# Performance work log

Measured on AMD Instinct MI355X. Metric: run time of the kernel, lower is better.

## Reference

```python
import jax, jax.numpy as jnp
import numpy as np

WINDOW = (7, 7)
SHIFT = (3, 3)
NUM_HEADS = 4
DIM = 128


def _rel_pos_index():
    wh, ww = WINDOW
    coords = np.stack(np.meshgrid(np.arange(wh), np.arange(ww), indexing='ij'))  # [2,wh,ww]
    cf = coords.reshape(2, -1)                    # [2, N]
    rc = (cf[:, :, None] - cf[:, None, :]).transpose(1, 2, 0)  # [N,N,2]
    rc[:, :, 0] += wh - 1
    rc[:, :, 1] += ww - 1
    rc[:, :, 0] *= 2 * ww - 1
    return jnp.asarray(rc.sum(-1).reshape(-1))    # [N*N] int


def _attn_mask_np(pH, pW, sh):
    # Static-shape shift mask (host-side numpy; constant under jit).
    wh, ww = WINDOW
    m = np.zeros((pH, pW))
    h_slices = ((0, pH - wh), (pH - wh, pH - sh[0]), (pH - sh[0], pH))
    w_slices = ((0, pW - ww), (pW - ww, pW - sh[1]), (pW - sh[1], pW))
    cnt = 0
    for hs in h_slices:
        for ws in w_slices:
            m[hs[0]:hs[1], ws[0]:ws[1]] = cnt
            cnt += 1
    m = m.reshape(pH // wh, wh, pW // ww, ww).transpose(0, 2, 1, 3).reshape(-1, wh * ww)
    diff = m[:, None, :] - m[:, :, None]          # [num_windows, N, N]
    return jnp.asarray(np.where(diff != 0, -100.0, 0.0), dtype=np.float32)


def setup_inputs() -> dict:
    key = jax.random.key(0)
    ks = jax.random.split(key, 9)
    B, H, W, C = 32, 56, 56, DIM
    return {
        'input_q': jax.random.normal(ks[0], (B, H, W, C), jnp.float32),
        'input_k': jax.random.normal(ks[1], (B, H, W, C), jnp.float32),
        'input_v': jax.random.normal(ks[2], (B, H, W, C), jnp.float32),
        'q_weight': jax.random.normal(ks[3], (C, C), jnp.float32) * 0.05,
        'q_bias': jnp.zeros((C,), jnp.float32),
        'k_weight': jax.random.normal(ks[4], (C, C), jnp.float32) * 0.05,
        'k_bias': jnp.zeros((C,), jnp.float32),
        'v_weight': jax.random.normal(ks[5], (C, C), jnp.float32) * 0.05,
        'v_bias': jnp.zeros((C,), jnp.float32),
        'proj_weight': jax.random.normal(ks[6], (C, C), jnp.float32) * 0.05,
        'proj_bias': jnp.zeros((C,), jnp.float32),
        'rpb_table': jax.random.normal(ks[7], ((2 * WINDOW[0] - 1) * (2 * WINDOW[1] - 1), NUM_HEADS), jnp.float32) * 0.02,
    }


def reference(input_q, input_k, input_v, q_weight, q_bias, k_weight, k_bias,
              v_weight, v_bias, proj_weight, proj_bias, rpb_table):
    B, H, W, C = input_q.shape
    wh, ww = WINDOW
    pad_b = (wh - H % wh) % wh
    pad_r = (ww - W % ww) % ww
    pad = lambda t: jnp.pad(t, ((0, 0), (0, pad_b), (0, pad_r), (0, 0)))
    qx, kx, vx = pad(input_q), pad(input_k), pad(input_v)
    pad_H, pad_W = H + pad_b, W + pad_r
    sh = [0 if wh >= pad_H else SHIFT[0], 0 if ww >= pad_W else SHIFT[1]]
    if sum(sh) > 0:
        roll = lambda t: jnp.roll(t, (-sh[0], -sh[1]), axis=(1, 2))
        qx, kx, vx = roll(qx), roll(kx), roll(vx)
    nWh, nWw = pad_H // wh, pad_W // ww
    num_windows = nWh * nWw
    N = wh * ww

    def part(t):  # [B,pH,pW,C] -> [B*num_windows, N, C]
        t = t.reshape(B, nWh, wh, nWw, ww, C).transpose(0, 1, 3, 2, 4, 5)
        return t.reshape(B * num_windows, N, C)

    qx, kx, vx = part(qx), part(kx), part(vx)
    hd = C // NUM_HEADS

    def heads(x, w, b):  # linear + split heads -> [BW, nH, N, hd]
        return (x @ w.T + b).reshape(-1, N, NUM_HEADS, hd).transpose(0, 2, 1, 3)

    q = heads(qx, q_weight, q_bias) * (hd ** -0.5)
    k = heads(kx, k_weight, k_bias)
    v = heads(vx, v_weight, v_bias)

    attn = jnp.einsum('whqd,whkd->whqk', q, k)    # [BW, nH, N, N]
    rpb = rpb_table[_rel_pos_index()].reshape(N, N, NUM_HEADS).transpose(2, 0, 1)[None]
    attn = attn + rpb
    if sum(sh) > 0:
        mask = _attn_mask_np(pad_H, pad_W, sh)    # [num_windows, N, N]
        attn = attn.reshape(B, num_windows, NUM_HEADS, N, N) + mask[None, :, None]
        attn = attn.reshape(B * num_windows, NUM_HEADS, N, N)
    attn = jax.nn.softmax(attn, axis=-1)

    x = jnp.einsum('whqk,whkd->whqd', attn, v).transpose(0, 2, 1, 3).reshape(B * num_windows, N, C)
    x = x @ proj_weight.T + proj_bias
    x = x.reshape(B, nWh, nWw, wh, ww, C).transpose(0, 1, 3, 2, 4, 5).reshape(B, pad_H, pad_W, C)
    if sum(sh) > 0:
        x = jnp.roll(x, (sh[0], sh[1]), axis=(1, 2))
    return x[:, :H, :W, :]
```

## Files before the change

kernel.cpp:

```cpp
#include <hip/hip_runtime.h>
#include <hip/hip_bf16.h>

typedef __attribute__((ext_vector_type(8))) short s16x8;
typedef __attribute__((ext_vector_type(4))) float f32x4;
typedef __attribute__((ext_vector_type(16))) float f32x16;
typedef __attribute__((ext_vector_type(2))) unsigned int u32x2;
typedef __attribute__((ext_vector_type(4))) unsigned int u32x4;

#define MFMA16(a, b, c) __builtin_amdgcn_mfma_f32_16x16x32_bf16((a), (b), (c), 0, 0, 0)
#define MFMA32(a, b, c) __builtin_amdgcn_mfma_f32_32x32x16_bf16((a), (b), (c), 0, 0, 0)
#define LOG2E 1.4426950408889634f

static __device__ __forceinline__ unsigned int pk2(float a, float b) {
  union { __hip_bfloat162 h2; unsigned int u; } cv;
  cv.h2 = __float22bfloat162_rn(make_float2(a, b));
  return cv.u;
}
static __device__ __forceinline__ int div7(int x) { return (x * 9363) >> 16; }
static __device__ __forceinline__ int swz256(int row, int byteoff) {
  return row * 256 + (byteoff ^ ((row & 7) << 4));
}
static __device__ __forceinline__ int swz128(int row, int byteoff) {
  return row * 128 + (byteoff ^ ((row & 7) << 4));
}

__global__ void swin_prep(const float* __restrict__ wq, const float* __restrict__ wk,
                          const float* __restrict__ wv, const float* __restrict__ wp,
                          const float* __restrict__ rpb_table,
                          unsigned short* __restrict__ wsW, float* __restrict__ rpbm) {
  int idx = blockIdx.x * 256 + threadIdx.x;
  if (idx < 65536) {
    int t = idx >> 14, loc = idx & 16383;
    const float* s = (t == 0) ? wq : (t == 1) ? wk : (t == 2) ? wv : wp;
    union { __hip_bfloat16 h; unsigned short u; } cv;
    cv.h = __float2bfloat16(s[loc]);
    wsW[idx] = cv.u;
  } else {
    int k = idx - 65536;
    int c = k >> 14;
    int h = (k >> 12) & 3;
    int i = (k >> 6) & 63, j = k & 63;
    float val;
    if (j >= 49) val = -1e30f;
    else if (i >= 49) val = 0.f;
    else {
      int yi = div7(i), xi = i - yi * 7;
      int yj = div7(j), xj = j - yj * 7;
      int ridx = (yi - yj + 6) * 13 + (xi - xj + 6);
      val = rpb_table[ridx * 4 + h];
      int cwi = c >> 1, cwj = c & 1;
      int rgi = (cwi ? (yi < 4 ? 3 : 6) : 0) + (cwj ? (xi < 4 ? 1 : 2) : 0);
      int rgj = (cwi ? (yj < 4 ? 3 : 6) : 0) + (cwj ? (xj < 4 ? 1 : 2) : 0);
      if (rgi != rgj) val -= 100.f;
      val *= LOG2E;
    }
    rpbm[k] = val;
  }
}

__global__ __launch_bounds__(512, 6) void swin_main(
    const float* __restrict__ xq, const float* __restrict__ xk, const float* __restrict__ xv,
    const float* __restrict__ bq, const float* __restrict__ bk, const float* __restrict__ bv,
    const float* __restrict__ bp, const unsigned short* __restrict__ wsW,
    const float* __restrict__ rpbm, float* __restrict__ out) {
  __shared__ __align__(16) char sm[49152];

  const int tid = threadIdx.x;
  const int lane = tid & 63;
  const int wv_ = tid >> 6;
  const int l15 = lane & 15;
  const int lg = lane >> 4;
  const int kgrp = lg * 8;
  const int rsub = lg * 4;
  const int l31 = lane & 31;
  const int hi = lane >> 5;

  const int bid = blockIdx.x;
  const int b = bid >> 6;
  const int widx = bid & 63;
  const int wi = widx >> 3, wj = widx & 7;
  const long obase = (long)b * 56 * 56 * 128;
  const int mcase = ((wi == 7) ? 2 : 0) + ((wj == 7) ? 1 : 0);

  const int xrow = tid >> 3;
  const int xk16 = (tid & 7) << 4;
  long xoff = -1;
  if (xrow < 49) {
    int ty = div7(xrow), tx = xrow - ty * 7;
    int ih = wi * 7 + ty + 3; if (ih >= 56) ih -= 56;
    int iw = wj * 7 + tx + 3; if (iw >= 56) iw -= 56;
    xoff = obase + (long)((ih * 56 + iw) * 128 + xk16);
  }
  float xr[16];
#pragma unroll
  for (int i = 0; i < 16; ++i) xr[i] = 0.f;

  auto issue_x = [&](const float* src) {
    if (xoff >= 0) {
      const float* p = src + xoff;
#pragma unroll
      for (int q = 0; q < 4; ++q) {
        f32x4 v = *(const f32x4*)(p + q * 4);
        xr[q * 4 + 0] = v[0]; xr[q * 4 + 1] = v[1];
        xr[q * 4 + 2] = v[2]; xr[q * 4 + 3] = v[3];
      }
    }
  };
  auto write_x = [&]() {
    unsigned int w[8];
#pragma unroll
    for (int i = 0; i < 8; ++i) w[i] = pk2(xr[2 * i], xr[2 * i + 1]);
    u32x4 a = {w[0], w[1], w[2], w[3]};
    u32x4 bb = {w[4], w[5], w[6], w[7]};
    *(u32x4*)(sm + swz256(xrow, xk16 * 2)) = a;
    *(u32x4*)(sm + swz256(xrow, xk16 * 2 + 16)) = bb;
  };

  auto linearT = [&](int woff, const float* bias, float scale, int dstbase) {
    const int nrow = wv_ * 16 + l15;
    s16x8 afr[4];
#pragma unroll
    for (int kt = 0; kt < 4; ++kt)
      afr[kt] = *(const s16x8*)(wsW + woff + nrow * 128 + kt * 32 + kgrp);
    f32x4 bv4 = *(const f32x4*)(bias + wv_ * 16 + rsub);
    float bb0 = bv4[0] * scale, bb1 = bv4[1] * scale;
    float bb2 = bv4[2] * scale, bb3 = bv4[3] * scale;
#pragma unroll
    for (int tt = 0; tt < 4; ++tt) {
      f32x4 acc = {0.f, 0.f, 0.f, 0.f};
#pragma unroll
      for (int kt = 0; kt < 4; ++kt) {
        s16x8 bfr = *(const s16x8*)(sm + swz256(tt * 16 + l15, (kt * 32 + kgrp) * 2));
        acc = MFMA16(afr[kt], bfr, acc);
      }
      u32x2 pkw = {pk2(acc[0] * scale + bb0, acc[1] * scale + bb1),
                   pk2(acc[2] * scale + bb2, acc[3] * scale + bb3)};
      *(u32x2*)(sm + dstbase + swz256(tt * 16 + l15, 2 * (wv_ * 16 + rsub))) = pkw;
    }
  };

  auto linearV = [&](int woff, const float* bias) {
    const int n = wv_ * 16 + l15;
    s16x8 bfr[4];
#pragma unroll
    for (int kt = 0; kt < 4; ++kt)
      bfr[kt] = *(const s16x8*)(wsW + woff + n * 128 + kt * 32 + kgrp);
    float bval = bias[n];
#pragma unroll
    for (int mt = 0; mt < 4; ++mt) {
      f32x4 acc = {0.f, 0.f, 0.f, 0.f};
#pragma unroll
      for (int kt = 0; kt < 4; ++kt) {
        s16x8 afr = *(const s16x8*)(sm + swz256(mt * 16 + l15, (kt * 32 + kgrp) * 2));
        acc = MFMA16(afr, bfr[kt], acc);
      }
      u32x2 pkw = {pk2(acc[0] + bval, acc[1] + bval), pk2(acc[2] + bval, acc[3] + bval)};
      *(u32x2*)(sm + 16384 + swz128(n, 2 * (mt * 16 + rsub))) = pkw;
    }
  };

  const float QSCALE = 0.17677669529663687f * LOG2E;

  issue_x(xq);
  write_x(); __syncthreads();
  issue_x(xk);
  linearT(0, bq, QSCALE, 16384); __syncthreads();
  write_x(); __syncthreads();
  issue_x(xv);
  linearT(16384, bk, 1.f, 32768); __syncthreads();
  write_x();

  const int h = wv_ & 3;
  const int half = wv_ >> 2;
  const int coff = h * 32;
  unsigned int pu[2][4][2];
  {
    s16x8 qfr[2], kfr[2][2];
#pragma unroll
    for (int s = 0; s < 2; ++s) {
      qfr[s] = *(const s16x8*)(sm + 16384 + swz256(half * 32 + l31, 2 * (coff + s * 16 + hi * 8)));
#pragma unroll
      for (int t = 0; t < 2; ++t)
        kfr[t][s] = *(const s16x8*)(sm + 32768 + swz256(t * 32 + l31, 2 * (coff + s * 16 + hi * 8)));
    }
    f32x16 S[2];
    S[0] = (f32x16)0.f; S[1] = (f32x16)0.f;
#pragma unroll
    for (int s = 0; s < 2; ++s) {
      S[0] = MFMA32(kfr[0][s], qfr[s], S[0]);
      S[1] = MFMA32(kfr[1][s], qfr[s], S[1]);
    }
    const float* rpbm_h = rpbm + (((mcase << 2) + h) << 12) + (half * 32 + l31) * 64 + 4 * hi;
#pragma unroll
    for (int t = 0; t < 2; ++t)
#pragma unroll
      for (int g = 0; g < 4; ++g) {
        f32x4 rv = *(const f32x4*)(rpbm_h + t * 32 + g * 8);
#pragma unroll
        for (int e = 0; e < 4; ++e) S[t][g * 4 + e] += rv[e];
      }
    float m = S[0][0];
#pragma unroll
    for (int t = 0; t < 2; ++t)
#pragma unroll
      for (int r = 0; r < 16; ++r) m = fmaxf(m, S[t][r]);
    m = fmaxf(m, __shfl_xor(m, 32));
    float sum = 0.f;
#pragma unroll
    for (int t = 0; t < 2; ++t)
#pragma unroll
      for (int r = 0; r < 16; ++r) { float e = exp2f(S[t][r] - m); S[t][r] = e; sum += e; }
    sum += __shfl_xor(sum, 32);
    float inv = 1.0f / sum;
#pragma unroll
    for (int t = 0; t < 2; ++t)
#pragma unroll
      for (int g = 0; g < 4; ++g) {
        pu[t][g][0] = pk2(S[t][g * 4 + 0] * inv, S[t][g * 4 + 1] * inv);
        pu[t][g][1] = pk2(S[t][g * 4 + 2] * inv, S[t][g * 4 + 3] * inv);
      }
  }
  __syncthreads();
  linearV(32768, bv);
  __syncthreads();

  {
    f32x16 O = (f32x16)0.f;
#pragma unroll
    for (int s = 0; s < 4; ++s) {
      const int t = s >> 1, gb = (s & 1) * 2;
      unsigned int own0 = pu[t][gb + hi][0], own1 = pu[t][gb + hi][1];
      unsigned int po0 = __shfl_xor(pu[t][gb + 1 - hi][0], 32);
      unsigned int po1 = __shfl_xor(pu[t][gb + 1 - hi][1], 32);
      union { u32x4 u; s16x8 s; } pf;
      pf.u = hi ? (u32x4){po0, po1, own0, own1} : (u32x4){own0, own1, po0, po1};
      s16x8 vfr = *(const s16x8*)(sm + 16384 + swz128(coff + l31, 2 * (s * 16 + hi * 8)));
      O = MFMA32(vfr, pf.s, O);
    }
#pragma unroll
    for (int g = 0; g < 4; ++g) {
      u32x2 w = {pk2(O[g * 4 + 0], O[g * 4 + 1]), pk2(O[g * 4 + 2], O[g * 4 + 3])};
      *(u32x2*)(sm + 32768 + swz256(half * 32 + l31, 2 * (coff + g * 8 + 4 * hi))) = w;
    }
  }
  __syncthreads();

  {
    const int nrow = wv_ * 16 + l15;
    s16x8 afr[4];
#pragma unroll
    for (int kt = 0; kt < 4; ++kt)
      afr[kt] = *(const s16x8*)(wsW + 49152 + nrow * 128 + kt * 32 + kgrp);
    f32x4 bv4 = *(const f32x4*)(bp + wv_ * 16 + rsub);
#pragma unroll
    for (int tt = 0; tt < 4; ++tt) {
      f32x4 acc = {0.f, 0.f, 0.f, 0.f};
#pragma unroll
      for (int kt = 0; kt < 4; ++kt) {
        s16x8 bfr = *(const s16x8*)(sm + 32768 + swz256(tt * 16 + l15, (kt * 32 + kgrp) * 2));
        acc = MFMA16(afr[kt], bfr, acc);
      }
      int tok = tt * 16 + l15;
      if (tok < 49) {
        int ty = div7(tok), tx = tok - ty * 7;
        int oh = wi * 7 + ty + 3; if (oh >= 56) oh -= 56;
        int ow = wj * 7 + tx + 3; if (ow >= 56) ow -= 56;
        f32x4 res = {acc[0] + bv4[0], acc[1] + bv4[1], acc[2] + bv4[2], acc[3] + bv4[3]};
        *(f32x4*)(out + obase + (oh * 56 + ow) * 128 + wv_ * 16 + rsub) = res;
      }
    }
  }
}

extern "C" void kernel_launch(void* const* d_in, const int* in_sizes, int n_in,
                              void* d_out, int out_size, void* d_ws, size_t ws_size,
                              hipStream_t stream) {
  const float* xq = (const float*)d_in[0];
  const float* xk = (const float*)d_in[1];
  const float* xv = (const float*)d_in[2];
  const float* wq = (const float*)d_in[3];
  const float* bq = (const float*)d_in[4];
  const float* wk = (const float*)d_in[5];
  const float* bk = (const float*)d_in[6];
  const float* wv = (const float*)d_in[7];
  const float* bv = (const float*)d_in[8];
  const float* wp = (const float*)d_in[9];
  const float* bp = (const float*)d_in[10];
  const float* rpb = (const float*)d_in[11];

  unsigned short* wsW = (unsigned short*)d_ws;
  float* rpbm = (float*)((char*)d_ws + 131072);

  swin_prep<<<512, 256, 0, stream>>>(wq, wk, wv, wp, rpb, wsW, rpbm);

  float* out = (float*)d_out;
  swin_main<<<2048, 512, 0, stream>>>(xq, xk, xv, bq, bk, bv, bp, wsW, rpbm, out);
}
```

Before: 87.01 us.

## Load Q/K/V inputs together and compute all projections before a single barrier

All three input tiles (q, k, v) are now loaded from global memory up front and staged into separate LDS regions, replacing the earlier sequence of load/project/sync per tensor. The three linear projections run back-to-back with their results held in registers, then are written to LDS after one barrier. The bias-table load is issued before the QK MFMA so it can seed the accumulator, and the V projection no longer sits between softmax and the PV product. This cuts the number of block-wide barriers and exposes more memory-level parallelism, at the cost of higher register pressure and possibly lower occupancy.

```diff
diff --git a/kernel.cpp b/kernel.cpp
--- a/kernel.cpp
+++ b/kernel.cpp
@@ -91,114 +91,149 @@
     int iw = wj * 7 + tx + 3; if (iw >= 56) iw -= 56;
     xoff = obase + (long)((ih * 56 + iw) * 128 + xk16);
   }
-  float xr[16];
-#pragma unroll
-  for (int i = 0; i < 16; ++i) xr[i] = 0.f;
-
-  auto issue_x = [&](const float* src) {
+  {
+    float ra[16], rb[16], rc[16];
+#pragma unroll
+    for (int i = 0; i < 16; ++i) { ra[i] = 0.f; rb[i] = 0.f; rc[i] = 0.f; }
     if (xoff >= 0) {
-      const float* p = src + xoff;
 #pragma unroll
       for (int q = 0; q < 4; ++q) {
-        f32x4 v = *(const f32x4*)(p + q * 4);
-        xr[q * 4 + 0] = v[0]; xr[q * 4 + 1] = v[1];
-        xr[q * 4 + 2] = v[2]; xr[q * 4 + 3] = v[3];
-      }
-    }
-  };
-  auto write_x = [&]() {
-    unsigned int w[8];
-#pragma unroll
-    for (int i = 0; i < 8; ++i) w[i] = pk2(xr[2 * i], xr[2 * i + 1]);
-    u32x4 a = {w[0], w[1], w[2], w[3]};
-    u32x4 bb = {w[4], w[5], w[6], w[7]};
-    *(u32x4*)(sm + swz256(xrow, xk16 * 2)) = a;
-    *(u32x4*)(sm + swz256(xrow, xk16 * 2 + 16)) = bb;
-  };
-
-  auto linearT = [&](int woff, const float* bias, float scale, int dstbase) {
+        f32x4 v = *(const f32x4*)(xq + xoff + q * 4);
+        ra[q*4+0]=v[0]; ra[q*4+1]=v[1]; ra[q*4+2]=v[2]; ra[q*4+3]=v[3];
+      }
+#pragma unroll
+      for (int q = 0; q < 4; ++q) {
+        f32x4 v = *(const f32x4*)(xk + xoff + q * 4);
+        rb[q*4+0]=v[0]; rb[q*4+1]=v[1]; rb[q*4+2]=v[2]; rb[q*4+3]=v[3];
+      }
+#pragma unroll
+      for (int q = 0; q < 4; ++q) {
+        f32x4 v = *(const f32x4*)(xv + xoff + q * 4);
+        rc[q*4+0]=v[0]; rc[q*4+1]=v[1]; rc[q*4+2]=v[2]; rc[q*4+3]=v[3];
+      }
+    }
+    auto wrx = [&](int base, float* r) {
+      unsigned int w[8];
+#pragma unroll
+      for (int i = 0; i < 8; ++i) w[i] = pk2(r[2*i], r[2*i+1]);
+      u32x4 a = {w[0], w[1], w[2], w[3]};
+      u32x4 bb = {w[4], w[5], w[6], w[7]};
+      *(u32x4*)(sm + base + swz256(xrow, xk16 * 2)) = a;
+      *(u32x4*)(sm + base + swz256(xrow, xk16 * 2 + 16)) = bb;
+    };
+    wrx(0, ra);
+    wrx(16384, rb);
+    wrx(32768, rc);
+  }
+  __syncthreads();
+
+  const float QSCALE = 0.17677669529663687f * LOG2E;
+  unsigned int qpk[4][2], kpk[4][2], vpk[4][2];
+  {
     const int nrow = wv_ * 16 + l15;
-    s16x8 afr[4];
-#pragma unroll
-    for (int kt = 0; kt < 4; ++kt)
-      afr[kt] = *(const s16x8*)(wsW + woff + nrow * 128 + kt * 32 + kgrp);
-    f32x4 bv4 = *(const f32x4*)(bias + wv_ * 16 + rsub);
-    float bb0 = bv4[0] * scale, bb1 = bv4[1] * scale;
-    float bb2 = bv4[2] * scale, bb3 = bv4[3] * scale;
-#pragma unroll
-    for (int tt = 0; tt < 4; ++tt) {
-      f32x4 acc = {0.f, 0.f, 0.f, 0.f};
-#pragma unroll
-      for (int kt = 0; kt < 4; ++kt) {
-        s16x8 bfr = *(const s16x8*)(sm + swz256(tt * 16 + l15, (kt * 32 + kgrp) * 2));
-        acc = MFMA16(afr[kt], bfr, acc);
-      }
-      u32x2 pkw = {pk2(acc[0] * scale + bb0, acc[1] * scale + bb1),
-                   pk2(acc[2] * scale + bb2, acc[3] * scale + bb3)};
-      *(u32x2*)(sm + dstbase + swz256(tt * 16 + l15, 2 * (wv_ * 16 + rsub))) = pkw;
-    }
-  };
-
-  auto linearV = [&](int woff, const float* bias) {
-    const int n = wv_ * 16 + l15;
-    s16x8 bfr[4];
-#pragma unroll
-    for (int kt = 0; kt < 4; ++kt)
-      bfr[kt] = *(const s16x8*)(wsW + woff + n * 128 + kt * 32 + kgrp);
-    float bval = bias[n];
-#pragma unroll
-    for (int mt = 0; mt < 4; ++mt) {
-      f32x4 acc = {0.f, 0.f, 0.f, 0.f};
-#pragma unroll
-      for (int kt = 0; kt < 4; ++kt) {
-        s16x8 afr = *(const s16x8*)(sm + swz256(mt * 16 + l15, (kt * 32 + kgrp) * 2));
-        acc = MFMA16(afr, bfr[kt], acc);
-      }
-      u32x2 pkw = {pk2(acc[0] + bval, acc[1] + bval), pk2(acc[2] + bval, acc[3] + bval)};
-      *(u32x2*)(sm + 16384 + swz128(n, 2 * (mt * 16 + rsub))) = pkw;
-    }
-  };
-
-  const float QSCALE = 0.17677669529663687f * LOG2E;
-
-  issue_x(xq);
-  write_x(); __syncthreads();
-  issue_x(xk);
-  linearT(0, bq, QSCALE, 16384); __syncthreads();
-  write_x(); __syncthreads();
-  issue_x(xv);
-  linearT(16384, bk, 1.f, 32768); __syncthreads();
-  write_x();
+    {
+      s16x8 afr[4];
+#pragma unroll
+      for (int kt = 0; kt < 4; ++kt)
+        afr[kt] = *(const s16x8*)(wsW + nrow * 128 + kt * 32 + kgrp);
+      f32x4 bv4 = *(const f32x4*)(bq + wv_ * 16 + rsub);
+#pragma unroll
+      for (int tt = 0; tt < 4; ++tt) {
+        f32x4 acc = {0.f, 0.f, 0.f, 0.f};
+#pragma unroll
+        for (int kt = 0; kt < 4; ++kt) {
+          s16x8 bfr = *(const s16x8*)(sm + swz256(tt * 16 + l15, (kt * 32 + kgrp) * 2));
+          acc = MFMA16(afr[kt], bfr, acc);
+        }
+        qpk[tt][0] = pk2(acc[0] * QSCALE + bv4[0] * QSCALE, acc[1] * QSCALE + bv4[1] * QSCALE);
+        qpk[tt][1] = pk2(acc[2] * QSCALE + bv4[2] * QSCALE, acc[3] * QSCALE + bv4[3] * QSCALE);
+      }
+    }
+    {
+      s16x8 afr[4];
+#pragma unroll
+      for (int kt = 0; kt < 4; ++kt)
+        afr[kt] = *(const s16x8*)(wsW + 16384 + nrow * 128 + kt * 32 + kgrp);
+      f32x4 bv4 = *(const f32x4*)(bk + wv_ * 16 + rsub);
+#pragma unroll
+      for (int tt = 0; tt < 4; ++tt) {
+        f32x4 acc = {0.f, 0.f, 0.f, 0.f};
+#pragma unroll
+        for (int kt = 0; kt < 4; ++kt) {
+          s16x8 bfr = *(const s16x8*)(sm + 16384 + swz256(tt * 16 + l15, (kt * 32 + kgrp) * 2));
+          acc = MFMA16(afr[kt], bfr, acc);
+        }
+        kpk[tt][0] = pk2(acc[0] + bv4[0], acc[1] + bv4[1]);
+        kpk[tt][1] = pk2(acc[2] + bv4[2], acc[3] + bv4[3]);
+      }
+    }
+    {
+      s16x8 bfrw[4];
+#pragma unroll
+      for (int kt = 0; kt < 4; ++kt)
+        bfrw[kt] = *(const s16x8*)(wsW + 32768 + nrow * 128 + kt * 32 + kgrp);
+      float bval = bv[nrow];
+#pragma unroll
+      for (int mt = 0; mt < 4; ++mt) {
+        f32x4 acc = {0.f, 0.f, 0.f, 0.f};
+#pragma unroll
+        for (int kt = 0; kt < 4; ++kt) {
+          s16x8 afr = *(const s16x8*)(sm + 32768 + swz256(mt * 16 + l15, (kt * 32 + kgrp) * 2));
+          acc = MFMA16(afr, bfrw[kt], acc);
+        }
+        vpk[mt][0] = pk2(acc[0] + bval, acc[1] + bval);
+        vpk[mt][1] = pk2(acc[2] + bval, acc[3] + bval);
+      }
+    }
+  }
+  __syncthreads();
+
+#pragma unroll
+  for (int tt = 0; tt < 4; ++tt) {
+    u32x2 w = {qpk[tt][0], qpk[tt][1]};
+    *(u32x2*)(sm + swz256(tt * 16 + l15, 2 * (wv_ * 16 + rsub))) = w;
+  }
+#pragma unroll
+  for (int tt = 0; tt < 4; ++tt) {
+    u32x2 w = {kpk[tt][0], kpk[tt][1]};
+    *(u32x2*)(sm + 16384 + swz256(tt * 16 + l15, 2 * (wv_ * 16 + rsub))) = w;
+  }
+#pragma unroll
+  for (int mt = 0; mt < 4; ++mt) {
+    u32x2 w = {vpk[mt][0], vpk[mt][1]};
+    *(u32x2*)(sm + 32768 + swz128(wv_ * 16 + l15, 2 * (mt * 16 + rsub))) = w;
+  }
+  __syncthreads();
 
   const int h = wv_ & 3;
   const int half = wv_ >> 2;
   const int coff = h * 32;
   unsigned int pu[2][4][2];
+  f32x16 O;
   {
+    const float* rpbm_h = rpbm + (((mcase << 2) + h) << 12) + (half * 32 + l31) * 64 + 4 * hi;
+    f32x16 S[2];
+#pragma unroll
+    for (int t = 0; t < 2; ++t)
+#pragma unroll
+      for (int g = 0; g < 4; ++g) {
+        f32x4 rv = *(const f32x4*)(rpbm_h + t * 32 + g * 8);
+        S[t][g*4+0] = rv[0]; S[t][g*4+1] = rv[1];
+        S[t][g*4+2] = rv[2]; S[t][g*4+3] = rv[3];
+      }
     s16x8 qfr[2], kfr[2][2];
 #pragma unroll
     for (int s = 0; s < 2; ++s) {
-      qfr[s] = *(const s16x8*)(sm + 16384 + swz256(half * 32 + l31, 2 * (coff + s * 16 + hi * 8)));
+      qfr[s] = *(const s16x8*)(sm + swz256(half * 32 + l31, 2 * (coff + s * 16 + hi * 8)));
 #pragma unroll
       for (int t = 0; t < 2; ++t)
-        kfr[t][s] = *(const s16x8*)(sm + 32768 + swz256(t * 32 + l31, 2 * (coff + s * 16 + hi * 8)));
-    }
-    f32x16 S[2];
-    S[0] = (f32x16)0.f; S[1] = (f32x16)0.f;
+        kfr[t][s] = *(const s16x8*)(sm + 16384 + swz256(t * 32 + l31, 2 * (coff + s * 16 + hi * 8)));
+    }
 #pragma unroll
     for (int s = 0; s < 2; ++s) {
       S[0] = MFMA32(kfr[0][s], qfr[s], S[0]);
       S[1] = MFMA32(kfr[1][s], qfr[s], S[1]);
     }
-    const float* rpbm_h = rpbm + (((mcase << 2) + h) << 12) + (half * 32 + l31) * 64 + 4 * hi;
-#pragma unroll
-    for (int t = 0; t < 2; ++t)
-#pragma unroll
-      for (int g = 0; g < 4; ++g) {
-        f32x4 rv = *(const f32x4*)(rpbm_h + t * 32 + g * 8);
-#pragma unroll
-        for (int e = 0; e < 4; ++e) S[t][g * 4 + e] += rv[e];
-      }
     float m = S[0][0];
 #pragma unroll
     for (int t = 0; t < 2; ++t)
@@ -216,16 +251,10 @@
     for (int t = 0; t < 2; ++t)
 #pragma unroll
       for (int g = 0; g < 4; ++g) {
-        pu[t][g][0] = pk2(S[t][g * 4 + 0] * inv, S[t][g * 4 + 1] * inv);
-        pu[t][g][1] = pk2(S[t][g * 4 + 2] * inv, S[t][g * 4 + 3] * inv);
-      }
-  }
-  __syncthreads();
-  linearV(32768, bv);
-  __syncthreads();
-
-  {
-    f32x16 O = (f32x16)0.f;
+        pu[t][g][0] = pk2(S[t][g*4+0] * inv, S[t][g*4+1] * inv);
+        pu[t][g][1] = pk2(S[t][g*4+2] * inv, S[t][g*4+3] * inv);
+      }
+    O = (f32x16)0.f;
 #pragma unroll
     for (int s = 0; s < 4; ++s) {
       const int t = s >> 1, gb = (s & 1) * 2;
@@ -234,14 +263,16 @@
       unsigned int po1 = __shfl_xor(pu[t][gb + 1 - hi][1], 32);
       union { u32x4 u; s16x8 s; } pf;
       pf.u = hi ? (u32x4){po0, po1, own0, own1} : (u32x4){own0, own1, po0, po1};
-      s16x8 vfr = *(const s16x8*)(sm + 16384 + swz128(coff + l31, 2 * (s * 16 + hi * 8)));
+      s16x8 vfr = *(const s16x8*)(sm + 32768 + swz128(coff + l31, 2 * (s * 16 + hi * 8)));
       O = MFMA32(vfr, pf.s, O);
     }
-#pragma unroll
-    for (int g = 0; g < 4; ++g) {
-      u32x2 w = {pk2(O[g * 4 + 0], O[g * 4 + 1]), pk2(O[g * 4 + 2], O[g * 4 + 3])};
-      *(u32x2*)(sm + 32768 + swz256(half * 32 + l31, 2 * (coff + g * 8 + 4 * hi))) = w;
-    }
+  }
+  __syncthreads();
+
+#pragma unroll
+  for (int g = 0; g < 4; ++g) {
+    u32x2 w = {pk2(O[g*4+0], O[g*4+1]), pk2(O[g*4+2], O[g*4+3])};
+    *(u32x2*)(sm + swz256(half * 32 + l31, 2 * (coff + g * 8 + 4 * hi))) = w;
   }
   __syncthreads();
 
@@ -257,7 +288,7 @@
       f32x4 acc = {0.f, 0.f, 0.f, 0.f};
 #pragma unroll
       for (int kt = 0; kt < 4; ++kt) {
-        s16x8 bfr = *(const s16x8*)(sm + 32768 + swz256(tt * 16 + l15, (kt * 32 + kgrp) * 2));
+        s16x8 bfr = *(const s16x8*)(sm + swz256(tt * 16 + l15, (kt * 32 + kgrp) * 2));
         acc = MFMA16(afr[kt], bfr, acc);
       }
       int tok = tt * 16 + l15;
```

Result: faster. 82.90 us (-4.7%).
